# Kernel tuning notes

Measured on AMD Instinct MI355X. Metric: run time of the kernel, lower is better.

## Reference

```python
import jax, jax.numpy as jnp
import numpy as np

N_NODES = 10000
N_EDGES = 320000
HIDDEN = 128
MIX = 8


def setup_inputs() -> dict:
    key = jax.random.key(0)
    k1, k2, k3, k4 = jax.random.split(key, 4)
    X = jax.random.normal(k1, (N_NODES, HIDDEN), dtype=jnp.float32)
    # nn.Linear default init scale ~ 1/sqrt(fan_in)
    W_A = jax.random.normal(k2, (HIDDEN, HIDDEN), dtype=jnp.float32) / np.sqrt(HIDDEN)
    W_B = jax.random.normal(k3, (MIX, HIDDEN), dtype=jnp.float32) / np.sqrt(HIDDEN)
    edge_index = jax.random.randint(k4, (2, N_EDGES), 0, N_NODES, dtype=jnp.int64)
    return {"X": X, "W_A": W_A, "W_B": W_B, "edge_index": edge_index, "num_nodes": N_NODES}


def reference(X, W_A, W_B, edge_index, num_nodes):
    src, dst = edge_index[0], edge_index[1]
    X_src = X[src]                                            # (E, h) gather
    # hyper-network weights per edge: W_B(gelu(W_A(x)))  -> (E, mix)
    W_tar_edge = jax.nn.gelu(X_src @ W_A.T, approximate=False) @ W_B.T
    # edge-wise outer product (E, h, mix)
    cross = X_src[:, :, None] * W_tar_edge[:, None, :]
    # scatter-add into node bins (N, h, mix)
    agg = jnp.zeros((num_nodes, X.shape[1], W_tar_edge.shape[1]), dtype=X.dtype)
    agg = agg.at[dst].add(cross)
    agg = jax.nn.gelu(agg, approximate=False)
    # gather back per edge and contract over mix dim -> (E, h)
    out_edge = jnp.einsum('ehm,em->eh', agg[dst], W_tar_edge)
    return (out_edge, src, dst)
```

## Files before the change

kernel.cpp:

```cpp
#include <hip/hip_runtime.h>

#define HIDDEN 128
#define MIX 8
#define CAP 128

#define NBW 32
#define LDX 33
#define KT  16
#define LDW 17
#define LDG 132

typedef float v2f __attribute__((ext_vector_type(2)));

__device__ __forceinline__ float gelu_exact(float x) {
    return 0.5f * x * (1.0f + erff(x * 0.7071067811865476f));
}

__global__ __launch_bounds__(256) void k_prep(const float* __restrict__ X,
                                              const float* __restrict__ W_A,
                                              const float* __restrict__ W_B,
                                              float* __restrict__ Wnode,
                                              const int* __restrict__ src,
                                              const int* __restrict__ dst,
                                              int* __restrict__ cursor,
                                              int2* __restrict__ bins,
                                              float* __restrict__ out_src,
                                              float* __restrict__ out_dst,
                                              int N, int E, int WB) {
    int t = threadIdx.x;

    if ((int)blockIdx.x >= WB) {
        int e = ((int)blockIdx.x - WB) * 256 + t;
        if (e < E) {
            int d = dst[e];
            int s = src[e];
            int p = atomicAdd(&cursor[d], 1);
            if (p < CAP) bins[(size_t)d * CAP + p] = make_int2(e, s);
            __builtin_nontemporal_store((float)s, &out_src[e]);
            __builtin_nontemporal_store((float)d, &out_dst[e]);
        }
        return;
    }

    __shared__ float xs[NBW * LDX];
    __shared__ float wa[HIDDEN * LDW];
    __shared__ float gsm[NBW * LDG];
    __shared__ float wb[MIX * LDG];

    int n0 = blockIdx.x * NBW;

    {
        int r = t >> 3;
        int c0 = (t & 7) * 16;
        int rn = n0 + r; if (rn >= N) rn = N - 1;
        const float* xp = X + (size_t)rn * HIDDEN + c0;
        float4 a = ((const float4*)xp)[0];
        float4 b = ((const float4*)xp)[1];
        float4 c = ((const float4*)xp)[2];
        float4 d = ((const float4*)xp)[3];
        float tmp[16] = {a.x,a.y,a.z,a.w, b.x,b.y,b.z,b.w,
                         c.x,c.y,c.z,c.w, d.x,d.y,d.z,d.w};
#pragma unroll
        for (int q = 0; q < 16; ++q) xs[r * LDX + c0 + q] = tmp[q];
    }

    int ngrp = t & 7;
    int jgrp = t >> 3;
    float acc[4][4];
#pragma unroll
    for (int i = 0; i < 4; ++i)
#pragma unroll
        for (int j = 0; j < 4; ++j) acc[i][j] = 0.f;

    for (int kt = 0; kt < HIDDEN; kt += KT) {
        __syncthreads();
        {
            int j = t >> 1;
            int c0 = (t & 1) * 8;
            const float* wp = W_A + (size_t)j * HIDDEN + kt + c0;
            float4 a = ((const float4*)wp)[0];
            float4 b = ((const float4*)wp)[1];
            float tmp[8] = {a.x,a.y,a.z,a.w, b.x,b.y,b.z,b.w};
#pragma unroll
            for (int q = 0; q < 8; ++q) wa[j * LDW + c0 + q] = tmp[q];
        }
        __syncthreads();
#pragma unroll
        for (int k = 0; k < KT; ++k) {
            float xv[4], wv[4];
#pragma unroll
            for (int i = 0; i < 4; ++i) xv[i] = xs[(ngrp * 4 + i) * LDX + kt + k];
#pragma unroll
            for (int j = 0; j < 4; ++j) wv[j] = wa[(jgrp * 4 + j) * LDW + k];
#pragma unroll
            for (int i = 0; i < 4; ++i)
#pragma unroll
                for (int j = 0; j < 4; ++j) acc[i][j] += xv[i] * wv[j];
        }
    }

#pragma unroll
    for (int i = 0; i < 4; ++i)
#pragma unroll
        for (int j = 0; j < 4; ++j)
            gsm[(ngrp * 4 + i) * LDG + (jgrp * 4 + j)] = gelu_exact(acc[i][j]);

    if (t < 64) {
        int r = t >> 3;
        int c0 = (t & 7) * 16;
        const float* wp = W_B + (size_t)r * HIDDEN + c0;
        float4 a = ((const float4*)wp)[0];
        float4 b = ((const float4*)wp)[1];
        float4 c = ((const float4*)wp)[2];
        float4 d = ((const float4*)wp)[3];
        float tmp[16] = {a.x,a.y,a.z,a.w, b.x,b.y,b.z,b.w,
                         c.x,c.y,c.z,c.w, d.x,d.y,d.z,d.w};
#pragma unroll
        for (int q = 0; q < 16; ++q) wb[r * LDG + c0 + q] = tmp[q];
    }
    __syncthreads();

    {
        int n = t >> 3;
        int m = t & 7;
        float a = 0.f;
#pragma unroll 8
        for (int k = 0; k < HIDDEN; ++k)
            a += gsm[n * LDG + k] * wb[m * LDG + k];
        if (n0 + n < N) Wnode[(size_t)n0 * MIX + t] = a;
    }
}

__global__ __launch_bounds__(256) void k_node(const float* __restrict__ X,
                                              const float* __restrict__ Wnode,
                                              const int2* __restrict__ bins,
                                              const int* __restrict__ cursor,
                                              float* __restrict__ out_edge,
                                              int N) {
    int lane = threadIdx.x & 63;
    int n = blockIdx.x * 4 + (threadIdx.x >> 6);
    if (n >= N) return;
    int cnt = cursor[n];
    if (cnt > CAP) cnt = CAP;
    if (cnt == 0) return;
    const int2* bp = bins + (size_t)n * CAP;

    float ag0[MIX], ag1[MIX];
#pragma unroll
    for (int m = 0; m < MIX; ++m) { ag0[m] = 0.f; ag1[m] = 0.f; }

    for (int c0 = 0; c0 < cnt; c0 += 64) {
        int nb = min(64, cnt - c0);
        int idx = c0 + ((lane < nb) ? lane : 0);
        int2 es = bp[idx];
        int s_l = es.y;
#pragma unroll 8
        for (int i = 0; i < nb; ++i) {
            int s = __builtin_amdgcn_readlane(s_l, i);
            const float* wp = Wnode + (size_t)s * MIX;
            float2 x = ((const float2*)(X + (size_t)s * HIDDEN))[lane];
#pragma unroll
            for (int m = 0; m < MIX; ++m) {
                float w = wp[m];
                ag0[m] += x.x * w;
                ag1[m] += x.y * w;
            }
        }
    }

#pragma unroll
    for (int m = 0; m < MIX; ++m) {
        ag0[m] = gelu_exact(ag0[m]);
        ag1[m] = gelu_exact(ag1[m]);
    }

    for (int c0 = 0; c0 < cnt; c0 += 64) {
        int nb = min(64, cnt - c0);
        int idx = c0 + ((lane < nb) ? lane : 0);
        int2 es = bp[idx];
        int e_l = es.x, s_l = es.y;
#pragma unroll 4
        for (int i = 0; i < nb; ++i) {
            int s = __builtin_amdgcn_readlane(s_l, i);
            int e = __builtin_amdgcn_readlane(e_l, i);
            const float* wp = Wnode + (size_t)s * MIX;
            v2f o;
            o.x = ag0[0]*wp[0] + ag0[1]*wp[1] + ag0[2]*wp[2] + ag0[3]*wp[3]
                + ag0[4]*wp[4] + ag0[5]*wp[5] + ag0[6]*wp[6] + ag0[7]*wp[7];
            o.y = ag1[0]*wp[0] + ag1[1]*wp[1] + ag1[2]*wp[2] + ag1[3]*wp[3]
                + ag1[4]*wp[4] + ag1[5]*wp[5] + ag1[6]*wp[6] + ag1[7]*wp[7];
            __builtin_nontemporal_store(o, (v2f*)(out_edge + (size_t)e * HIDDEN) + lane);
        }
    }
}

extern "C" void kernel_launch(void* const* d_in, const int* in_sizes, int n_in,
                              void* d_out, int out_size, void* d_ws, size_t ws_size,
                              hipStream_t stream) {
    const float* X   = (const float*)d_in[0];
    const float* W_A = (const float*)d_in[1];
    const float* W_B = (const float*)d_in[2];
    const int*   ei  = (const int*)d_in[3];

    const int N = in_sizes[0] / HIDDEN;
    const int E = in_sizes[3] / 2;
    const int* src = ei;
    const int* dst = ei + E;

    float* out      = (float*)d_out;
    float* out_edge = out;
    float* out_src  = out + (size_t)E * HIDDEN;
    float* out_dst  = out_src + E;

    int*  cursor = (int*)d_ws;
    int2* bins   = (int2*)(cursor + N);
    float* Wnode = (float*)(bins + (size_t)N * CAP);

    hipMemsetAsync(cursor, 0, sizeof(int) * (size_t)N, stream);

    int WB = (N + NBW - 1) / NBW;
    int EB = (E + 255) / 256;

    k_prep<<<WB + EB, 256, 0, stream>>>(X, W_A, W_B, Wnode, src, dst,
                                        cursor, bins, out_src, out_dst, N, E, WB);
    k_node<<<(N + 3) / 4, 256, 0, stream>>>(X, Wnode, bins, cursor, out_edge, N);
}
```

Before: 245.7 us.

## Fuse memset, prep and node kernels into one cooperative persistent kernel

Replaces the memset plus two kernel launches with a single cooperative kernel that uses grid-wide syncs between the cursor reset, the node-weight/binning phase and the per-node aggregation phase. Blocks become persistent and loop over edges and nodes with grid strides. Shared memory is unioned to cut LDS use and raise occupancy. The aim is to remove launch overheads and tail gaps, at the cost of grid.sync latency and less parallelism in the edge binning phase; if the cooperative launch fails it falls back to the old kernels.

```diff
diff --git a/kernel.cpp b/kernel.cpp
--- a/kernel.cpp
+++ b/kernel.cpp
@@ -1,4 +1,7 @@
 #include <hip/hip_runtime.h>
+#include <hip/hip_cooperative_groups.h>
+
+namespace cg = cooperative_groups;
 
 #define HIDDEN 128
 #define MIX 8
@@ -14,6 +17,187 @@
 
 __device__ __forceinline__ float gelu_exact(float x) {
     return 0.5f * x * (1.0f + erff(x * 0.7071067811865476f));
+}
+
+__global__ __launch_bounds__(256) void k_fused(
+        const float* __restrict__ X,
+        const float* __restrict__ W_A,
+        const float* __restrict__ W_B,
+        const int* __restrict__ src,
+        const int* __restrict__ dst,
+        float* __restrict__ Wnode,
+        int* __restrict__ cursor,
+        int2* __restrict__ bins,
+        float* __restrict__ out_src,
+        float* __restrict__ out_dst,
+        float* __restrict__ out_edge,
+        int N, int E, int WB) {
+    cg::grid_group grid = cg::this_grid();
+    int t = threadIdx.x;
+    int b = blockIdx.x;
+    int G = gridDim.x;
+
+    __shared__ union SmemU {
+        struct { float xs[NBW * LDX]; float wa[HIDDEN * LDW]; } ab;
+        float gsm[NBW * LDG];
+    } u;
+    __shared__ float wb[MIX * LDG];
+
+    for (int i = b * 256 + t; i < N; i += G * 256) cursor[i] = 0;
+    grid.sync();
+
+    if (b < WB) {
+        int n0 = b * NBW;
+
+        {
+            int r = t >> 3;
+            int c0 = (t & 7) * 16;
+            int rn = n0 + r; if (rn >= N) rn = N - 1;
+            const float* xp = X + (size_t)rn * HIDDEN + c0;
+            float4 a = ((const float4*)xp)[0];
+            float4 bb = ((const float4*)xp)[1];
+            float4 c = ((const float4*)xp)[2];
+            float4 d = ((const float4*)xp)[3];
+            float tmp[16] = {a.x,a.y,a.z,a.w, bb.x,bb.y,bb.z,bb.w,
+                             c.x,c.y,c.z,c.w, d.x,d.y,d.z,d.w};
+#pragma unroll
+            for (int q = 0; q < 16; ++q) u.ab.xs[r * LDX + c0 + q] = tmp[q];
+        }
+
+        int ngrp = t & 7;
+        int jgrp = t >> 3;
+        float acc[4][4];
+#pragma unroll
+        for (int i = 0; i < 4; ++i)
+#pragma unroll
+            for (int j = 0; j < 4; ++j) acc[i][j] = 0.f;
+
+        for (int kt = 0; kt < HIDDEN; kt += KT) {
+            __syncthreads();
+            {
+                int j = t >> 1;
+                int c0 = (t & 1) * 8;
+                const float* wp = W_A + (size_t)j * HIDDEN + kt + c0;
+                float4 a = ((const float4*)wp)[0];
+                float4 bb = ((const float4*)wp)[1];
+                float tmp[8] = {a.x,a.y,a.z,a.w, bb.x,bb.y,bb.z,bb.w};
+#pragma unroll
+                for (int q = 0; q < 8; ++q) u.ab.wa[j * LDW + c0 + q] = tmp[q];
+            }
+            __syncthreads();
+#pragma unroll
+            for (int k = 0; k < KT; ++k) {
+                float xv[4], wv[4];
+#pragma unroll
+                for (int i = 0; i < 4; ++i) xv[i] = u.ab.xs[(ngrp * 4 + i) * LDX + kt + k];
+#pragma unroll
+                for (int j = 0; j < 4; ++j) wv[j] = u.ab.wa[(jgrp * 4 + j) * LDW + k];
+#pragma unroll
+                for (int i = 0; i < 4; ++i)
+#pragma unroll
+                    for (int j = 0; j < 4; ++j) acc[i][j] += xv[i] * wv[j];
+            }
+        }
+        __syncthreads();
+
+#pragma unroll
+        for (int i = 0; i < 4; ++i)
+#pragma unroll
+            for (int j = 0; j < 4; ++j)
+                u.gsm[(ngrp * 4 + i) * LDG + (jgrp * 4 + j)] = gelu_exact(acc[i][j]);
+
+        if (t < 64) {
+            int r = t >> 3;
+            int c0 = (t & 7) * 16;
+            const float* wp = W_B + (size_t)r * HIDDEN + c0;
+            float4 a = ((const float4*)wp)[0];
+            float4 bb = ((const float4*)wp)[1];
+            float4 c = ((const float4*)wp)[2];
+            float4 d = ((const float4*)wp)[3];
+            float tmp[16] = {a.x,a.y,a.z,a.w, bb.x,bb.y,bb.z,bb.w,
+                             c.x,c.y,c.z,c.w, d.x,d.y,d.z,d.w};
+#pragma unroll
+            for (int q = 0; q < 16; ++q) wb[r * LDG + c0 + q] = tmp[q];
+        }
+        __syncthreads();
+
+        {
+            int n = t >> 3;
+            int m = t & 7;
+            float a = 0.f;
+#pragma unroll 8
+            for (int k = 0; k < HIDDEN; ++k)
+                a += u.gsm[n * LDG + k] * wb[m * LDG + k];
+            if (n0 + n < N) Wnode[(size_t)n0 * MIX + t] = a;
+        }
+    } else {
+        for (int e = (b - WB) * 256 + t; e < E; e += (G - WB) * 256) {
+            int d = dst[e];
+            int s = src[e];
+            int p = atomicAdd(&cursor[d], 1);
+            if (p < CAP) bins[(size_t)d * CAP + p] = make_int2(e, s);
+            __builtin_nontemporal_store((float)s, &out_src[e]);
+            __builtin_nontemporal_store((float)d, &out_dst[e]);
+        }
+    }
+    grid.sync();
+
+    int lane = t & 63;
+    int wid = t >> 6;
+    for (int n = b * 4 + wid; n < N; n += G * 4) {
+        int cnt = cursor[n];
+        if (cnt > CAP) cnt = CAP;
+        if (cnt == 0) continue;
+        const int2* bp = bins + (size_t)n * CAP;
+
+        float ag0[MIX], ag1[MIX];
+#pragma unroll
+        for (int m = 0; m < MIX; ++m) { ag0[m] = 0.f; ag1[m] = 0.f; }
+
+        for (int c0 = 0; c0 < cnt; c0 += 64) {
+            int nb = min(64, cnt - c0);
+            int idx = c0 + ((lane < nb) ? lane : 0);
+            int2 es = bp[idx];
+            int s_l = es.y;
+#pragma unroll 8
+            for (int i = 0; i < nb; ++i) {
+                int s = __builtin_amdgcn_readlane(s_l, i);
+                const float* wp = Wnode + (size_t)s * MIX;
+                float2 x = ((const float2*)(X + (size_t)s * HIDDEN))[lane];
+#pragma unroll
+                for (int m = 0; m < MIX; ++m) {
+                    float w = wp[m];
+                    ag0[m] += x.x * w;
+                    ag1[m] += x.y * w;
+                }
+            }
+        }
+
+#pragma unroll
+        for (int m = 0; m < MIX; ++m) {
+            ag0[m] = gelu_exact(ag0[m]);
+            ag1[m] = gelu_exact(ag1[m]);
+        }
+
+        for (int c0 = 0; c0 < cnt; c0 += 64) {
+            int nb = min(64, cnt - c0);
+            int idx = c0 + ((lane < nb) ? lane : 0);
+            int2 es = bp[idx];
+            int e_l = es.x, s_l = es.y;
+#pragma unroll 4
+            for (int i = 0; i < nb; ++i) {
+                int s = __builtin_amdgcn_readlane(s_l, i);
+                int e = __builtin_amdgcn_readlane(e_l, i);
+                const float* wp = Wnode + (size_t)s * MIX;
+                v2f o;
+                o.x = ag0[0]*wp[0] + ag0[1]*wp[1] + ag0[2]*wp[2] + ag0[3]*wp[3]
+                    + ag0[4]*wp[4] + ag0[5]*wp[5] + ag0[6]*wp[6] + ag0[7]*wp[7];
+                o.y = ag1[0]*wp[0] + ag1[1]*wp[1] + ag1[2]*wp[2] + ag1[3]*wp[3]
+                    + ag1[4]*wp[4] + ag1[5]*wp[5] + ag1[6]*wp[6] + ag1[7]*wp[7];
+                __builtin_nontemporal_store(o, (v2f*)(out_edge + (size_t)e * HIDDEN) + lane);
+            }
+        }
+    }
 }
 
 __global__ __launch_bounds__(256) void k_prep(const float* __restrict__ X,
@@ -28,7 +212,6 @@
                                               float* __restrict__ out_dst,
                                               int N, int E, int WB) {
     int t = threadIdx.x;
-
     if ((int)blockIdx.x >= WB) {
         int e = ((int)blockIdx.x - WB) * 256 + t;
         if (e < E) {
@@ -41,29 +224,26 @@
         }
         return;
     }
-
-    __shared__ float xs[NBW * LDX];
-    __shared__ float wa[HIDDEN * LDW];
-    __shared__ float gsm[NBW * LDG];
+    __shared__ union SmemU {
+        struct { float xs[NBW * LDX]; float wa[HIDDEN * LDW]; } ab;
+        float gsm[NBW * LDG];
+    } u;
     __shared__ float wb[MIX * LDG];
-
     int n0 = blockIdx.x * NBW;
-
     {
         int r = t >> 3;
         int c0 = (t & 7) * 16;
         int rn = n0 + r; if (rn >= N) rn = N - 1;
         const float* xp = X + (size_t)rn * HIDDEN + c0;
         float4 a = ((const float4*)xp)[0];
-        float4 b = ((const float4*)xp)[1];
+        float4 bb = ((const float4*)xp)[1];
         float4 c = ((const float4*)xp)[2];
         float4 d = ((const float4*)xp)[3];
-        float tmp[16] = {a.x,a.y,a.z,a.w, b.x,b.y,b.z,b.w,
+        float tmp[16] = {a.x,a.y,a.z,a.w, bb.x,bb.y,bb.z,bb.w,
                          c.x,c.y,c.z,c.w, d.x,d.y,d.z,d.w};
 #pragma unroll
-        for (int q = 0; q < 16; ++q) xs[r * LDX + c0 + q] = tmp[q];
-    }
-
+        for (int q = 0; q < 16; ++q) u.ab.xs[r * LDX + c0 + q] = tmp[q];
+    }
     int ngrp = t & 7;
     int jgrp = t >> 3;
     float acc[4][4];
@@ -71,7 +251,6 @@
     for (int i = 0; i < 4; ++i)
 #pragma unroll
         for (int j = 0; j < 4; ++j) acc[i][j] = 0.f;
-
     for (int kt = 0; kt < HIDDEN; kt += KT) {
         __syncthreads();
         {
@@ -79,54 +258,52 @@
             int c0 = (t & 1) * 8;
             const float* wp = W_A + (size_t)j * HIDDEN + kt + c0;
             float4 a = ((const float4*)wp)[0];
-            float4 b = ((const float4*)wp)[1];
-            float tmp[8] = {a.x,a.y,a.z,a.w, b.x,b.y,b.z,b.w};
-#pragma unroll
-            for (int q = 0; q < 8; ++q) wa[j * LDW + c0 + q] = tmp[q];
+            float4 bb = ((const float4*)wp)[1];
+            float tmp[8] = {a.x,a.y,a.z,a.w, bb.x,bb.y,bb.z,bb.w};
+#pragma unroll
+            for (int q = 0; q < 8; ++q) u.ab.wa[j * LDW + c0 + q] = tmp[q];
         }
         __syncthreads();
 #pragma unroll
         for (int k = 0; k < KT; ++k) {
             float xv[4], wv[4];
 #pragma unroll
-            for (int i = 0; i < 4; ++i) xv[i] = xs[(ngrp * 4 + i) * LDX + kt + k];
-#pragma unroll
-            for (int j = 0; j < 4; ++j) wv[j] = wa[(jgrp * 4 + j) * LDW + k];
+            for (int i = 0; i < 4; ++i) xv[i] = u.ab.xs[(ngrp * 4 + i) * LDX + kt + k];
+#pragma unroll
+            for (int j = 0; j < 4; ++j) wv[j] = u.ab.wa[(jgrp * 4 + j) * LDW + k];
 #pragma unroll
             for (int i = 0; i < 4; ++i)
 #pragma unroll
                 for (int j = 0; j < 4; ++j) acc[i][j] += xv[i] * wv[j];
         }
     }
-
+    __syncthreads();
 #pragma unroll
     for (int i = 0; i < 4; ++i)
 #pragma unroll
         for (int j = 0; j < 4; ++j)
-            gsm[(ngrp * 4 + i) * LDG + (jgrp * 4 + j)] = gelu_exact(acc[i][j]);
-
+            u.gsm[(ngrp * 4 + i) * LDG + (jgrp * 4 + j)] = gelu_exact(acc[i][j]);
     if (t < 64) {
         int r = t >> 3;
         int c0 = (t & 7) * 16;
         const float* wp = W_B + (size_t)r * HIDDEN + c0;
         float4 a = ((const float4*)wp)[0];
-        float4 b = ((const float4*)wp)[1];
+        float4 bb = ((const float4*)wp)[1];
         float4 c = ((const float4*)wp)[2];
         float4 d = ((const float4*)wp)[3];
-        float tmp[16] = {a.x,a.y,a.z,a.w, b.x,b.y,b.z,b.w,
+        float tmp[16] = {a.x,a.y,a.z,a.w, bb.x,bb.y,bb.z,bb.w,
                          c.x,c.y,c.z,c.w, d.x,d.y,d.z,d.w};
 #pragma unroll
         for (int q = 0; q < 16; ++q) wb[r * LDG + c0 + q] = tmp[q];
     }
     __syncthreads();
-
     {
         int n = t >> 3;
         int m = t & 7;
         float a = 0.f;
 #pragma unroll 8
         for (int k = 0; k < HIDDEN; ++k)
-            a += gsm[n * LDG + k] * wb[m * LDG + k];
+            a += u.gsm[n * LDG + k] * wb[m * LDG + k];
         if (n0 + n < N) Wnode[(size_t)n0 * MIX + t] = a;
     }
 }
@@ -144,11 +321,9 @@
     if (cnt > CAP) cnt = CAP;
     if (cnt == 0) return;
     const int2* bp = bins + (size_t)n * CAP;
-
     float ag0[MIX], ag1[MIX];
 #pragma unroll
     for (int m = 0; m < MIX; ++m) { ag0[m] = 0.f; ag1[m] = 0.f; }
-
     for (int c0 = 0; c0 < cnt; c0 += 64) {
         int nb = min(64, cnt - c0);
         int idx = c0 + ((lane < nb) ? lane : 0);
@@ -167,13 +342,11 @@
             }
         }
     }
-
 #pragma unroll
     for (int m = 0; m < MIX; ++m) {
         ag0[m] = gelu_exact(ag0[m]);
         ag1[m] = gelu_exact(ag1[m]);
     }
-
     for (int c0 = 0; c0 < cnt; c0 += 64) {
         int nb = min(64, cnt - c0);
         int idx = c0 + ((lane < nb) ? lane : 0);
@@ -202,8 +375,8 @@
     const float* W_B = (const float*)d_in[2];
     const int*   ei  = (const int*)d_in[3];
 
-    const int N = in_sizes[0] / HIDDEN;
-    const int E = in_sizes[3] / 2;
+    int N = in_sizes[0] / HIDDEN;
+    int E = in_sizes[3] / 2;
     const int* src = ei;
     const int* dst = ei + E;
 
@@ -216,12 +389,33 @@
     int2* bins   = (int2*)(cursor + N);
     float* Wnode = (float*)(bins + (size_t)N * CAP);
 
-    hipMemsetAsync(cursor, 0, sizeof(int) * (size_t)N, stream);
-
     int WB = (N + NBW - 1) / NBW;
     int EB = (E + 255) / 256;
 
-    k_prep<<<WB + EB, 256, 0, stream>>>(X, W_A, W_B, Wnode, src, dst,
-                                        cursor, bins, out_src, out_dst, N, E, WB);
-    k_node<<<(N + 3) / 4, 256, 0, stream>>>(X, Wnode, bins, cursor, out_edge, N);
+    static int g_grid = 0;
+    if (g_grid == 0) {
+        int bpc = 0;
+        hipOccupancyMaxActiveBlocksPerMultiprocessor(&bpc, k_fused, 256, 0);
+        int ncu = 0;
+        hipDeviceProp_t prop;
+        if (hipGetDeviceProperties(&prop, 0) == hipSuccess)
+            ncu = prop.multiProcessorCount;
+        if (ncu <= 0) ncu = 256;
+        if (bpc <= 0) bpc = 1;
+        g_grid = bpc * ncu;
+        if (g_grid <= WB) g_grid = WB + 256;
+    }
+
+    void* args[] = {(void*)&X, (void*)&W_A, (void*)&W_B, (void*)&src, (void*)&dst,
+                    (void*)&Wnode, (void*)&cursor, (void*)&bins,
+                    (void*)&out_src, (void*)&out_dst, (void*)&out_edge,
+                    (void*)&N, (void*)&E, (void*)&WB};
+    hipError_t err = hipLaunchCooperativeKernel((void*)k_fused, dim3(g_grid),
+                                                dim3(256), args, 0, stream);
+    if (err != hipSuccess) {
+        hipMemsetAsync(cursor, 0, sizeof(int) * (size_t)N, stream);
+        k_prep<<<WB + EB, 256, 0, stream>>>(X, W_A, W_B, Wnode, src, dst,
+                                            cursor, bins, out_src, out_dst, N, E, WB);
+        k_node<<<(N + 3) / 4, 256, 0, stream>>>(X, Wnode, bins, cursor, out_edge, N);
+    }
 }
```

After: 433.6 us. 76.5% more time.
